# Optimization experiments

Hardware: AMD Instinct MI355X
Metric: run time of the kernel (lower is better)

## Reference

```python
import jax, jax.numpy as jnp
import numpy as np

C = 64          # number of concepts (output_size)
MC = 100        # num_monte_carlo
TRI = C * (C + 1) // 2
ROWS, COLS = np.tril_indices(C)          # static lower-triangular indices
DIAG_MASK = ROWS == COLS                 # positions in c_sigma that are diagonal
DIAG = np.arange(C)


def setup_inputs() -> dict:
    key = jax.random.key(0)
    k_x, k_eps, k_wmu, k_wsig = jax.random.split(key, 4)
    B, F = 4096, 512
    return {
        "x": jax.random.normal(k_x, (B, F), jnp.float32),
        "eps": jax.random.normal(k_eps, (B, C, MC), jnp.float32),  # MVN standard-normal draws
        "w_mu": jax.random.normal(k_wmu, (C, F), jnp.float32) / np.float32(np.sqrt(F)),
        "b_mu": jnp.zeros((C,), jnp.float32),
        # sigma.weight.data *= 0.01 in the original module
        "w_sigma": jax.random.normal(k_wsig, (TRI, F), jnp.float32) * np.float32(0.01 / np.sqrt(F)),
        "b_sigma": jnp.zeros((TRI,), jnp.float32),
    }


def reference(x, eps, w_mu, b_mu, w_sigma, b_sigma):
    # mu head: Linear(F -> C)
    c_mu = x @ w_mu.T + b_mu                          # [B, C]
    # sigma head: Linear(F -> C*(C+1)/2)
    c_sigma = x @ w_sigma.T + b_sigma                 # [B, TRI]

    B = x.shape[0]
    # build lower-triangular scale matrix (predict_sigma)
    L = jnp.zeros((B, C, C), x.dtype)
    L = L.at[:, ROWS, COLS].set(c_sigma)
    diag_vals = jax.nn.softplus(c_sigma[:, DIAG_MASK]) + 1e-6
    L = L.at[:, DIAG, DIAG].set(diag_vals)            # [B, C, C]

    # MVN rsample([MC]) with scale_tril L: sample = mu + L @ eps
    logits = c_mu[:, :, None] + jnp.einsum('bij,bjm->bim', L, eps)  # [B, C, MC]
    return jax.nn.sigmoid(logits)
```

## Files before the change

kernel.cpp:

```cpp
#include <hip/hip_runtime.h>
#include <hip/hip_bf16.h>


typedef short bf16x8 __attribute__((ext_vector_type(8)));
typedef float f32x4 __attribute__((ext_vector_type(4)));

__device__ __forceinline__ unsigned short f2bf(float f) {
    union { float f; unsigned u; } u; u.f = f;
    unsigned r = u.u + 0x7FFFu + ((u.u >> 16) & 1u);
    return (unsigned short)(r >> 16);
}

__device__ __forceinline__ int swz(int r) { return (r ^ (r >> 3)) & 7; }

__device__ __forceinline__ void tri_ij(int t, int& i, int& j) {
    i = (int)((sqrtf((float)(8 * t + 1)) - 1.0f) * 0.5f);
    if ((i + 1) * (i + 2) / 2 <= t) ++i;
    if (i * (i + 1) / 2 > t) --i;
    j = t - ((i * (i + 1)) >> 1);
}

__device__ __forceinline__ void gload16(const void* g, void* l) {
    __builtin_amdgcn_global_load_lds(
        (const __attribute__((address_space(1))) void*)g,
        (__attribute__((address_space(3))) void*)l, 16, 0, 0);
}

__global__ __launch_bounds__(256) void cvt_kernel(
    const float* __restrict__ x, const float* __restrict__ wmu,
    const float* __restrict__ wsig,
    unsigned short* __restrict__ Xb, unsigned short* __restrict__ Wb) {
    const int NX = (4096 * 512) / 4;
    const int NW = (2144 * 512) / 4;
    const int NMU = (64 * 512) / 4;
    int tot = NX + NW;
    for (int i = blockIdx.x * blockDim.x + threadIdx.x; i < tot;
         i += gridDim.x * blockDim.x) {
        float4 v; unsigned short* dst;
        if (i < NX) {
            v = ((const float4*)x)[i];
            dst = Xb + (size_t)i * 4;
        } else {
            int j = i - NX;
            if (j < NMU) v = ((const float4*)wmu)[j];
            else         v = ((const float4*)wsig)[j - NMU];
            dst = Wb + (size_t)j * 4;
        }
        ushort4 o;
        o.x = f2bf(v.x); o.y = f2bf(v.y); o.z = f2bf(v.z); o.w = f2bf(v.w);
        *(ushort4*)dst = o;
    }
}

__global__ __launch_bounds__(256) void gemm_kernel(
    const unsigned short* __restrict__ Xb, const unsigned short* __restrict__ Wb,
    const float* __restrict__ bmu, const float* __restrict__ bsig,
    float* __restrict__ Mu, unsigned short* __restrict__ Sg) {
    __shared__ __align__(16) unsigned short smem[16384];

    int flat = blockIdx.y * 17 + blockIdx.x;
    int virt = (flat & 7) * 68 + (flat >> 3);
    int vbx = virt % 17, vby = virt / 17;
    int r0 = vby * 128, c0 = vbx * 128;

    int tid = threadIdx.x;
    int w = tid >> 6, lane = tid & 63;
    int wr = w >> 1, wc = w & 1;
    int lr = lane & 15, kg = lane >> 4;

    int sr = tid >> 3;
    int sc = tid & 7;
    int scx = sc ^ (sr & 7);
    const unsigned short* Ag = Xb + (size_t)(r0 + sr) * 512 + scx * 8;
    const unsigned short* Bg = Wb + (size_t)(c0 + sr) * 512 + scx * 8;
    unsigned short* As = smem + tid * 8;
    unsigned short* Bs = smem + 8192 + tid * 8;

    f32x4 acc[4][4];
    #pragma unroll
    for (int i = 0; i < 4; ++i)
        #pragma unroll
        for (int j = 0; j < 4; ++j) acc[i][j] = (f32x4){0.f, 0.f, 0.f, 0.f};

    for (int kt = 0; kt < 8; ++kt) {
        int k0 = kt * 64;
        #pragma unroll
        for (int i = 0; i < 4; ++i) {
            gload16(Ag + (size_t)i * 32 * 512 + k0, As + i * 2048);
            gload16(Bg + (size_t)i * 32 * 512 + k0, Bs + i * 2048);
        }
        __syncthreads();
        #pragma unroll
        for (int h = 0; h < 2; ++h) {
            bf16x8 a[4], bv[4];
            #pragma unroll
            for (int i = 0; i < 4; ++i) {
                int row = wr * 64 + i * 16 + lr;
                int ch = ((h << 2) | kg) ^ (row & 7);
                a[i] = *(const bf16x8*)(smem + row * 64 + ch * 8);
            }
            #pragma unroll
            for (int j = 0; j < 4; ++j) {
                int row = wc * 64 + j * 16 + lr;
                int ch = ((h << 2) | kg) ^ (row & 7);
                bv[j] = *(const bf16x8*)(smem + 8192 + row * 64 + ch * 8);
            }
            #pragma unroll
            for (int i = 0; i < 4; ++i)
                #pragma unroll
                for (int j = 0; j < 4; ++j)
                    acc[i][j] = __builtin_amdgcn_mfma_f32_16x16x32_bf16(
                        a[i], bv[j], acc[i][j], 0, 0, 0);
        }
        __syncthreads();
    }

    int rbase = r0 + wr * 64 + (kg << 2);
    #pragma unroll
    for (int j = 0; j < 4; ++j) {
        int col = c0 + wc * 64 + j * 16 + lr;
        if (col < 64) {
            float bias = bmu[col];
            #pragma unroll
            for (int i = 0; i < 4; ++i)
                #pragma unroll
                for (int r = 0; r < 4; ++r)
                    Mu[(size_t)(rbase + i * 16 + r) * 64 + col] = acc[i][j][r] + bias;
        } else if (col < 2144) {
            int t = col - 64;
            float bias = bsig[t];
            int ti, tj; tri_ij(t, ti, tj);
            bool dg = (tj == ti);
            #pragma unroll
            for (int i = 0; i < 4; ++i) {
                #pragma unroll
                for (int r = 0; r < 4; ++r) {
                    float v = acc[i][j][r] + bias;
                    if (dg) v = (v > 15.f ? v : __logf(1.f + __expf(v))) + 1e-6f;
                    Sg[(size_t)(rbase + i * 16 + r) * 2080 + t] = f2bf(v);
                }
            }
        }
    }
}

__global__ __launch_bounds__(256) void sample_kernel(
    const float* __restrict__ Mu, const unsigned short* __restrict__ Sg,
    const float* __restrict__ eps, float* __restrict__ out) {
    __shared__ __align__(16) unsigned short Lh[64][64];
    __shared__ __align__(16) unsigned short Ep[4][32][64];

    int b = blockIdx.x;
    int tid = threadIdx.x;
    int w = tid >> 6;
    int lane = tid & 63;
    int M0 = w << 5;
    const float* er = eps + (size_t)b * 6400;

    int ntask = (w < 3) ? 128 : 16;
    #pragma unroll
    for (int it = 0; it < 2; ++it) {
        int task = it * 64 + lane;
        if (task < ntask) {
            int mq = (w < 3) ? (task & 7) : 0;
            int kq = (w < 3) ? (task >> 3) : task;
            const float* p = er + kq * 400 + M0 + (mq << 2);
            float4 v0 = *(const float4*)(p);
            float4 v1 = *(const float4*)(p + 100);
            float4 v2 = *(const float4*)(p + 200);
            float4 v3 = *(const float4*)(p + 300);
            #pragma unroll
            for (int s = 0; s < 4; ++s) {
                int m = M0 + (mq << 2) + s;
                __hip_bfloat162 h0 = __float22bfloat162_rn(
                    make_float2(((const float*)&v0)[s], ((const float*)&v1)[s]));
                __hip_bfloat162 h1 = __float22bfloat162_rn(
                    make_float2(((const float*)&v2)[s], ((const float*)&v3)[s]));
                uint2 u; u.x = *(unsigned*)&h0; u.y = *(unsigned*)&h1;
                int chunk = (kq >> 1) ^ swz(m);
                *(uint2*)&Ep[w][m - M0][(chunk << 3) | ((kq & 1) << 2)] = u;
            }
        }
    }

    const unsigned short* sgu = Sg + (size_t)b * 2080;
    #pragma unroll
    for (int k = 0; k < 8; ++k) {
        int idx = tid + (k << 8);
        int i = idx >> 5;
        int j0 = (idx & 31) << 1;
        unsigned u = 0u;
        if (j0 <= i) {
            int t = ((i * (i + 1)) >> 1) + j0;
            u = sgu[t];
            if (j0 + 1 <= i) u |= ((unsigned)sgu[t + 1]) << 16;
        }
        *(unsigned*)&Lh[i][(((j0 >> 3) ^ swz(i)) << 3) | (j0 & 7)] = u;
    }

    int lr = lane & 15, kg = lane >> 4;
    float muv[4];
    #pragma unroll
    for (int g = 0; g < 4; ++g) muv[g] = Mu[(b << 6) + g * 16 + lr];

    __syncthreads();

    bf16x8 Lf0[4], Lf1[4];
    #pragma unroll
    for (int g = 0; g < 4; ++g) {
        int i = g * 16 + lr;
        int si = swz(i);
        Lf0[g] = *(const bf16x8*)&Lh[i][(kg ^ si) << 3];
        Lf1[g] = *(const bf16x8*)&Lh[i][((kg + 4) ^ si) << 3];
    }

    int ntile = (w < 3) ? 2 : 1;
    for (int tt = 0; tt < ntile; ++tt) {
        int mt = (w < 3) ? (2 * w + tt) : 6;
        int m = (mt << 4) + lr;
        int lm = m - M0;
        int sm = swz(m);
        bf16x8 a0 = *(const bf16x8*)&Ep[w][lm][(kg ^ sm) << 3];
        bf16x8 a1 = *(const bf16x8*)&Ep[w][lm][((kg + 4) ^ sm) << 3];
        int m0 = (mt << 4) + (kg << 2);
        #pragma unroll
        for (int g = 0; g < 4; ++g) {
            f32x4 acc = {0.f, 0.f, 0.f, 0.f};
            acc = __builtin_amdgcn_mfma_f32_16x16x32_bf16(a0, Lf0[g], acc, 0, 0, 0);
            acc = __builtin_amdgcn_mfma_f32_16x16x32_bf16(a1, Lf1[g], acc, 0, 0, 0);
            if (m0 < 100) {
                float4 o;
                #pragma unroll
                for (int r = 0; r < 4; ++r) {
                    float z = muv[g] + acc[r];
                    ((float*)&o)[r] = __fdividef(1.f, 1.f + __expf(-z));
                }
                *(float4*)(out + ((size_t)b * 64 + g * 16 + lr) * 100 + m0) = o;
            }
        }
    }
}

extern "C" void kernel_launch(void* const* d_in, const int* in_sizes, int n_in,
                              void* d_out, int out_size, void* d_ws, size_t ws_size,
                              hipStream_t stream) {
    const float* x    = (const float*)d_in[0];
    const float* eps  = (const float*)d_in[1];
    const float* wmu  = (const float*)d_in[2];
    const float* bmu  = (const float*)d_in[3];
    const float* wsig = (const float*)d_in[4];
    const float* bsig = (const float*)d_in[5];
    float* out = (float*)d_out;

    char* ws = (char*)d_ws;
    unsigned short* Xb = (unsigned short*)ws;
    unsigned short* Wb = (unsigned short*)(ws + 4194304);
    float*          Mu = (float*)(ws + 4194304 + 2195456);
    unsigned short* Sg = (unsigned short*)(ws + 4194304 + 2195456 + 1048576);

    cvt_kernel<<<2048, 256, 0, stream>>>(x, wmu, wsig, Xb, Wb);
    gemm_kernel<<<dim3(17, 32), 256, 0, stream>>>(Xb, Wb, bmu, bsig, Mu, Sg);
    sample_kernel<<<4096, 256, 0, stream>>>(Mu, Sg, eps, out);
}
```

Before: 85.69 us.

## Widen sample kernel to 512 threads and stage output through LDS for coalesced stores

The sample kernel now runs 512 threads per batch row, so each of seven waves handles one 16-wide Monte Carlo tile. The eps load is flattened across 400 threads. Sigmoid results are written into a swizzled LDS buffer that aliases the L/eps staging area, then stored to global memory as contiguous float4 rows. This replaces the strided per-lane output writes with coalesced stores. The cost is two extra block barriers and one idle wave in the compute phase.

```diff
diff --git a/kernel.cpp b/kernel.cpp
--- a/kernel.cpp
+++ b/kernel.cpp
@@ -144,49 +144,47 @@
     }
 }
 
-__global__ __launch_bounds__(256) void sample_kernel(
+__global__ __launch_bounds__(512, 8) void sample_kernel(
     const float* __restrict__ Mu, const unsigned short* __restrict__ Sg,
     const float* __restrict__ eps, float* __restrict__ out) {
-    __shared__ __align__(16) unsigned short Lh[64][64];
-    __shared__ __align__(16) unsigned short Ep[4][32][64];
+    __shared__ __align__(16) union {
+        struct {
+            unsigned short Lh[64][64];
+            unsigned short Ep[112][64];
+        } s;
+        float Ost[64][128];
+    } sm;
 
     int b = blockIdx.x;
     int tid = threadIdx.x;
     int w = tid >> 6;
     int lane = tid & 63;
-    int M0 = w << 5;
     const float* er = eps + (size_t)b * 6400;
 
-    int ntask = (w < 3) ? 128 : 16;
-    #pragma unroll
-    for (int it = 0; it < 2; ++it) {
-        int task = it * 64 + lane;
-        if (task < ntask) {
-            int mq = (w < 3) ? (task & 7) : 0;
-            int kq = (w < 3) ? (task >> 3) : task;
-            const float* p = er + kq * 400 + M0 + (mq << 2);
-            float4 v0 = *(const float4*)(p);
-            float4 v1 = *(const float4*)(p + 100);
-            float4 v2 = *(const float4*)(p + 200);
-            float4 v3 = *(const float4*)(p + 300);
-            #pragma unroll
-            for (int s = 0; s < 4; ++s) {
-                int m = M0 + (mq << 2) + s;
-                __hip_bfloat162 h0 = __float22bfloat162_rn(
-                    make_float2(((const float*)&v0)[s], ((const float*)&v1)[s]));
-                __hip_bfloat162 h1 = __float22bfloat162_rn(
-                    make_float2(((const float*)&v2)[s], ((const float*)&v3)[s]));
-                uint2 u; u.x = *(unsigned*)&h0; u.y = *(unsigned*)&h1;
-                int chunk = (kq >> 1) ^ swz(m);
-                *(uint2*)&Ep[w][m - M0][(chunk << 3) | ((kq & 1) << 2)] = u;
-            }
+    if (tid < 400) {
+        int mq = tid % 25, kq = tid / 25;
+        const float* p = er + kq * 400 + mq * 4;
+        float4 v0 = *(const float4*)(p);
+        float4 v1 = *(const float4*)(p + 100);
+        float4 v2 = *(const float4*)(p + 200);
+        float4 v3 = *(const float4*)(p + 300);
+        #pragma unroll
+        for (int s = 0; s < 4; ++s) {
+            int m = (mq << 2) + s;
+            __hip_bfloat162 h0 = __float22bfloat162_rn(
+                make_float2(((const float*)&v0)[s], ((const float*)&v1)[s]));
+            __hip_bfloat162 h1 = __float22bfloat162_rn(
+                make_float2(((const float*)&v2)[s], ((const float*)&v3)[s]));
+            uint2 u; u.x = *(unsigned*)&h0; u.y = *(unsigned*)&h1;
+            int chunk = (kq >> 1) ^ swz(m);
+            *(uint2*)&sm.s.Ep[m][(chunk << 3) | ((kq & 1) << 2)] = u;
         }
     }
 
     const unsigned short* sgu = Sg + (size_t)b * 2080;
     #pragma unroll
-    for (int k = 0; k < 8; ++k) {
-        int idx = tid + (k << 8);
+    for (int k = 0; k < 4; ++k) {
+        int idx = tid + (k << 9);
         int i = idx >> 5;
         int j0 = (idx & 31) << 1;
         unsigned u = 0u;
@@ -195,7 +193,7 @@
             u = sgu[t];
             if (j0 + 1 <= i) u |= ((unsigned)sgu[t + 1]) << 16;
         }
-        *(unsigned*)&Lh[i][(((j0 >> 3) ^ swz(i)) << 3) | (j0 & 7)] = u;
+        *(unsigned*)&sm.s.Lh[i][(((j0 >> 3) ^ swz(i)) << 3) | (j0 & 7)] = u;
     }
 
     int lr = lane & 15, kg = lane >> 4;
@@ -205,38 +203,53 @@
 
     __syncthreads();
 
-    bf16x8 Lf0[4], Lf1[4];
-    #pragma unroll
-    for (int g = 0; g < 4; ++g) {
-        int i = g * 16 + lr;
-        int si = swz(i);
-        Lf0[g] = *(const bf16x8*)&Lh[i][(kg ^ si) << 3];
-        Lf1[g] = *(const bf16x8*)&Lh[i][((kg + 4) ^ si) << 3];
-    }
-
-    int ntile = (w < 3) ? 2 : 1;
-    for (int tt = 0; tt < ntile; ++tt) {
-        int mt = (w < 3) ? (2 * w + tt) : 6;
-        int m = (mt << 4) + lr;
-        int lm = m - M0;
-        int sm = swz(m);
-        bf16x8 a0 = *(const bf16x8*)&Ep[w][lm][(kg ^ sm) << 3];
-        bf16x8 a1 = *(const bf16x8*)&Ep[w][lm][((kg + 4) ^ sm) << 3];
-        int m0 = (mt << 4) + (kg << 2);
+    bf16x8 Lf0[4], Lf1[4], a0, a1;
+    if (w < 7) {
+        #pragma unroll
+        for (int g = 0; g < 4; ++g) {
+            int i = g * 16 + lr;
+            int si = swz(i);
+            Lf0[g] = *(const bf16x8*)&sm.s.Lh[i][(kg ^ si) << 3];
+            Lf1[g] = *(const bf16x8*)&sm.s.Lh[i][((kg + 4) ^ si) << 3];
+        }
+        int m = (w << 4) + lr;
+        int smz = swz(m);
+        a0 = *(const bf16x8*)&sm.s.Ep[m][(kg ^ smz) << 3];
+        a1 = *(const bf16x8*)&sm.s.Ep[m][((kg + 4) ^ smz) << 3];
+    }
+
+    __syncthreads();
+
+    if (w < 7) {
+        int m0 = (w << 4) + (kg << 2);
         #pragma unroll
         for (int g = 0; g < 4; ++g) {
             f32x4 acc = {0.f, 0.f, 0.f, 0.f};
             acc = __builtin_amdgcn_mfma_f32_16x16x32_bf16(a0, Lf0[g], acc, 0, 0, 0);
             acc = __builtin_amdgcn_mfma_f32_16x16x32_bf16(a1, Lf1[g], acc, 0, 0, 0);
             if (m0 < 100) {
+                int n = g * 16 + lr;
                 float4 o;
                 #pragma unroll
                 for (int r = 0; r < 4; ++r) {
                     float z = muv[g] + acc[r];
                     ((float*)&o)[r] = __fdividef(1.f, 1.f + __expf(-z));
                 }
-                *(float4*)(out + ((size_t)b * 64 + g * 16 + lr) * 100 + m0) = o;
-            }
+                *(float4*)&sm.Ost[n][m0 ^ ((n & 7) << 2)] = o;
+            }
+        }
+    }
+
+    __syncthreads();
+
+    #pragma unroll
+    for (int k = 0; k < 4; ++k) {
+        int f = tid + (k << 9);
+        if (f < 1600) {
+            int row = f / 25;
+            int c4 = (f % 25) << 2;
+            float4 v = *(const float4*)&sm.Ost[row][c4 ^ ((row & 7) << 2)];
+            *(float4*)(out + ((size_t)b * 64 + row) * 100 + c4) = v;
         }
     }
 }
@@ -260,5 +273,5 @@
 
     cvt_kernel<<<2048, 256, 0, stream>>>(x, wmu, wsig, Xb, Wb);
     gemm_kernel<<<dim3(17, 32), 256, 0, stream>>>(Xb, Wb, bmu, bsig, Mu, Sg);
-    sample_kernel<<<4096, 256, 0, stream>>>(Mu, Sg, eps, out);
-}
+    sample_kernel<<<4096, 512, 0, stream>>>(Mu, Sg, eps, out);
+}
```

New measurement: 79.84 us. 6.8% less time.
